# Kernel optimization log

Measured on AMD Instinct MI355X. Metric: run time of the kernel, lower is better.

The kernel has to match this reference:

```python
import jax, jax.numpy as jnp
import numpy as np

E = 8          # num experts
TOPK = 2
D = 1024       # emb_size (expert hidden == emb_size)


def setup_inputs() -> dict:
    key = jax.random.key(0)
    ks = jax.random.split(key, 8)
    s = 1.0 / np.sqrt(D)
    x = jax.random.normal(ks[0], (4, 1024, D), dtype=jnp.float32)
    gate_W = jax.random.uniform(ks[1], (E, D), jnp.float32, -s, s)   # torch Linear weight (out,in)
    gate_b = jax.random.uniform(ks[2], (E,), jnp.float32, -s, s)
    w1 = jax.random.uniform(ks[3], (E, D, D), jnp.float32, -s, s)    # per-expert first Linear (out,in)
    b1 = jax.random.uniform(ks[4], (E, D), jnp.float32, -s, s)
    w2 = jax.random.uniform(ks[5], (E, D, D), jnp.float32, -s, s)    # per-expert second Linear (out,in)
    b2 = jax.random.uniform(ks[6], (E, D), jnp.float32, -s, s)
    return {"x": x, "gate_W": gate_W, "gate_b": gate_b,
            "w1": w1, "b1": b1, "w2": w2, "b2": b2}


def reference(x, gate_W, gate_b, w1, b1, w2, b2):
    x_shape = x.shape
    xt = x.reshape(-1, x_shape[-1])                       # [N, D]

    # gating
    gate_logits = xt @ gate_W.T + gate_b                  # [N, E]
    gate_prob = jax.nn.softmax(gate_logits, axis=-1)      # [N, E]
    top_w, top_i = jax.lax.top_k(gate_prob, TOPK)         # [N, K]
    top_w = jax.nn.softmax(top_w, axis=-1)                # renormalize over top-k

    # dense per-expert MLP: h = relu(x @ W1^T + b1); o = h @ W2^T + b2
    h = jax.nn.relu(jnp.einsum('nd,ehd->neh', xt, w1) + b1[None])   # [N, E, D]
    o = jnp.einsum('neh,eoh->neo', h, w2) + b2[None]                # [N, E, D]

    # gather top-k expert outputs per token and combine with weights
    o_top = jnp.take_along_axis(o, top_i[:, :, None], axis=1)       # [N, K, D]
    y = jnp.sum(o_top * top_w[:, :, None], axis=1)                  # [N, D]

    return y.reshape(x_shape), gate_prob
```

## Files before the change

### kernel.cpp

```cpp
#include <hip/hip_runtime.h>

#define NTOK 4096
#define DIM 1024
#define NE 8
#define NPAIR (NTOK * 2)

typedef __bf16 bf16x8 __attribute__((ext_vector_type(8)));
typedef float floatx4 __attribute__((ext_vector_type(4)));

__device__ __forceinline__ unsigned short f2bf(float f) {
  unsigned u = __float_as_uint(f);
  u = u + 0x7fffu + ((u >> 16) & 1u);
  return (unsigned short)(u >> 16);
}
__device__ __forceinline__ float bf2f(unsigned short h) {
  return __uint_as_float(((unsigned)h) << 16);
}

__device__ __forceinline__ void gld_lds16(const unsigned short* g, unsigned short* l) {
  __builtin_amdgcn_global_load_lds(
      (const __attribute__((address_space(1))) void*)g,
      (__attribute__((address_space(3))) void*)l, 16, 0, 0);
}

__global__ __launch_bounds__(256) void gate_kernel(
    const float* __restrict__ x, const float* __restrict__ gW,
    const float* __restrict__ gb,
    float* __restrict__ gp_out, int2* __restrict__ tops,
    float* __restrict__ pairw, int* __restrict__ cnt, int* __restrict__ done,
    unsigned short* __restrict__ x_bf)
{
  const int tid = threadIdx.x;
  if (blockIdx.x == 0) {
    if (tid < NE) cnt[tid] = 0;
    if (tid == NE) *done = 0;
  }
  const int lane = tid & 63;
  const int wid = tid >> 6;
  const int t = blockIdx.x * 4 + wid;

  float4 xv[4];
#pragma unroll
  for (int j = 0; j < 4; j++)
    xv[j] = ((const float4*)(x + (size_t)t * DIM))[lane + 64 * j];

#pragma unroll
  for (int j = 0; j < 4; j++) {
    ushort4 o;
    o.x = f2bf(xv[j].x); o.y = f2bf(xv[j].y);
    o.z = f2bf(xv[j].z); o.w = f2bf(xv[j].w);
    ((ushort4*)(x_bf + (size_t)t * DIM))[lane + 64 * j] = o;
  }

  float p[NE];
#pragma unroll
  for (int e = 0; e < NE; e++) {
    const float4* gwe = (const float4*)(gW + e * DIM);
    float s = 0.f;
#pragma unroll
    for (int j = 0; j < 4; j++) {
      float4 g = gwe[lane + 64 * j];
      s += xv[j].x * g.x + xv[j].y * g.y + xv[j].z * g.z + xv[j].w * g.w;
    }
    p[e] = s;
  }
#pragma unroll
  for (int e = 0; e < NE; e++) {
#pragma unroll
    for (int off = 32; off >= 1; off >>= 1) p[e] += __shfl_xor(p[e], off);
  }

  float m = -1e30f;
#pragma unroll
  for (int e = 0; e < NE; e++) { p[e] += gb[e]; m = fmaxf(m, p[e]); }
  float s = 0.f;
  float pr[NE];
#pragma unroll
  for (int e = 0; e < NE; e++) { pr[e] = __expf(p[e] - m); s += pr[e]; }
  float inv = 1.f / s;
#pragma unroll
  for (int e = 0; e < NE; e++) pr[e] *= inv;

  if (lane < NE) gp_out[(size_t)t * NE + lane] = pr[lane];

  if (lane == 0) {
    int i0 = 0;
#pragma unroll
    for (int e = 1; e < NE; e++) if (pr[e] > pr[i0]) i0 = e;
    int i1 = (i0 == 0) ? 1 : 0;
#pragma unroll
    for (int e = 0; e < NE; e++) if (e != i0 && pr[e] > pr[i1]) i1 = e;
    float d = __expf(pr[i1] - pr[i0]);
    float w0 = 1.f / (1.f + d);
    tops[t] = make_int2(i0, i1);
    pairw[t * 2] = w0;
    pairw[t * 2 + 1] = 1.f - w0;
  }
}

__global__ __launch_bounds__(256) void bin_sched_kernel(
    const int2* __restrict__ tops, int* __restrict__ cnt,
    int* __restrict__ bucket,
    int* __restrict__ posmap,
    int* __restrict__ done, int* __restrict__ base,
    int* __restrict__ sched, int* __restrict__ sched_n)
{
  const int t = blockIdx.x * 256 + threadIdx.x;
  const int lane = threadIdx.x & 63;
  int2 ti = tops[t];
#pragma unroll
  for (int slot = 0; slot < 2; slot++) {
    int e = slot ? ti.y : ti.x;
#pragma unroll
    for (int ex = 0; ex < NE; ex++) {
      bool mine = (e == ex);
      unsigned long long mask = __ballot(mine);
      if (mask) {
        int leader = __ffsll((long long)mask) - 1;
        int total = __popcll(mask);
        int prefix = __popcll(mask & ((1ull << lane) - 1ull));
        int idx = 0;
        if (lane == leader) idx = atomicAdd(&cnt[ex], total);
        idx = __shfl(idx, leader) + prefix;
        if (mine) {
          bucket[ex * NTOK + idx] = t * 2 + slot;
          posmap[t * 2 + slot] = (ex << 16) | idx;
        }
      }
    }
  }
  __syncthreads();
  if (threadIdx.x == 0) {
    if (atomicAdd(done, 1) == gridDim.x - 1) {
      int b = 0, pos = 0;
      for (int e = 0; e < NE; e++) {
        int c = atomicAdd(&cnt[e], 0);
        base[e] = b;
        int tiles = (c + 127) >> 7;
        for (int i = 0; i < tiles; i++) {
          int valid = c - i * 128; if (valid > 128) valid = 128;
          sched[pos++] = (e << 20) | (i << 8) | valid;
        }
        b += c;
      }
      base[NE] = b;
      *sched_n = pos;
    }
  }
}

__global__ __launch_bounds__(256) void cvt2_kernel(
    const float4* __restrict__ src1, ushort4* __restrict__ dst1,
    const float4* __restrict__ src2, ushort4* __restrict__ dst2, int half_blocks)
{
  int b = blockIdx.x;
  const float4* src = src1;
  ushort4* dst = dst1;
  if (b >= half_blocks) { b -= half_blocks; src = src2; dst = dst2; }
  const int i = b * 256 + threadIdx.x;
  float4 v = src[i];
  ushort4 o;
  o.x = f2bf(v.x); o.y = f2bf(v.y); o.z = f2bf(v.z); o.w = f2bf(v.w);
  dst[i] = o;
}

template <int RELU, int GATHER>
__global__ __launch_bounds__(512) void ffn_gemm(
    const unsigned short* __restrict__ A,
    const unsigned short* __restrict__ B,
    const float* __restrict__ bias,
    const int* __restrict__ base,
    const int* __restrict__ bucket,
    const int* __restrict__ sched, const int* __restrict__ sched_n,
    unsigned short* __restrict__ Out)
{
  const int l = blockIdx.x;
  const int xcd = l & 7;
  const int w = l >> 3;
  const int nt = w & 7;
  const int slot = xcd * 9 + (w >> 3);
  if (slot >= *sched_n) return;
  const int se = sched[slot];
  const int e = se >> 20;
  const int mt = (se >> 8) & 0xfff;
  const int valid = se & 255;
  const int arow0 = base[e] + mt * 128;

  __shared__ unsigned short lda[128 * 64];
  __shared__ unsigned short ldb[128 * 64];

  const int tid = threadIdx.x;
  const int lane = tid & 63;
  const int wid = tid >> 6;

  const unsigned short* ap[2];
  const unsigned short* bp[2];
#pragma unroll
  for (int j = 0; j < 2; j++) {
    int g = wid * 2 + j;
    int row = g * 8 + (lane >> 3);
    int gran = (lane & 7) ^ (row & 7);
    if (GATHER) {
      int idx = mt * 128 + row;
      int ce = base[e + 1] - base[e];
      if (idx > ce - 1) idx = ce - 1;
      int tok = bucket[e * NTOK + idx] >> 1;
      ap[j] = A + (size_t)tok * DIM + (gran << 3);
    } else {
      int prow = arow0 + row;
      if (prow > NPAIR - 1) prow = NPAIR - 1;
      ap[j] = A + (size_t)prow * DIM + (gran << 3);
    }
    bp[j] = B + ((size_t)e * DIM + nt * 128 + row) * DIM + (gran << 3);
  }

  floatx4 acc[4][2] = {};
  const int wm = (wid & 1) * 64;
  const int wn = (wid >> 1) * 32;
  const int quad = lane >> 4;
  const int cl = lane & 15;
  const int sw = cl & 7;

  for (int k0 = 0; k0 < 16; k0++) {
#pragma unroll
    for (int j = 0; j < 2; j++) {
      gld_lds16(ap[j], &lda[(wid * 2 + j) * 512]);
      gld_lds16(bp[j], &ldb[(wid * 2 + j) * 512]);
      ap[j] += 64;
      bp[j] += 64;
    }
    __syncthreads();
#pragma unroll
    for (int kk = 0; kk < 64; kk += 32) {
      const int gb = (kk >> 3) + quad;
      const int goff = ((gb ^ sw) << 3);
      bf16x8 af[4], bfr[2];
#pragma unroll
      for (int mi = 0; mi < 4; mi++)
        af[mi] = *(const bf16x8*)&lda[(wm + mi * 16 + cl) * 64 + goff];
#pragma unroll
      for (int ni = 0; ni < 2; ni++)
        bfr[ni] = *(const bf16x8*)&ldb[(wn + ni * 16 + cl) * 64 + goff];
#pragma unroll
      for (int mi = 0; mi < 4; mi++)
#pragma unroll
        for (int ni = 0; ni < 2; ni++)
          acc[mi][ni] = __builtin_amdgcn_mfma_f32_16x16x32_bf16(af[mi], bfr[ni], acc[mi][ni], 0, 0, 0);
    }
    if (k0 < 15) __syncthreads();
  }

#pragma unroll
  for (int ni = 0; ni < 2; ni++) {
    int col = nt * 128 + wn + ni * 16 + cl;
    float bval = bias[e * DIM + col];
#pragma unroll
    for (int mi = 0; mi < 4; mi++) {
#pragma unroll
      for (int reg = 0; reg < 4; reg++) {
        int rl = wm + mi * 16 + quad * 4 + reg;
        if (rl < valid) {
          float v = acc[mi][ni][reg] + bval;
          if (RELU) v = fmaxf(v, 0.f);
          Out[(size_t)(arow0 + rl) * DIM + col] = f2bf(v);
        }
      }
    }
  }
}

__global__ __launch_bounds__(256) void combine_kernel(
    const unsigned short* __restrict__ o, const int* __restrict__ posmap,
    const int* __restrict__ base, const float* __restrict__ pairw,
    float* __restrict__ y)
{
  const int t = blockIdx.x;
  const int tid = threadIdx.x;
  const int pm0 = posmap[t * 2], pm1 = posmap[t * 2 + 1];
  const int p0 = base[pm0 >> 16] + (pm0 & 0xffff);
  const int p1 = base[pm1 >> 16] + (pm1 & 0xffff);
  const float w0 = pairw[t * 2], w1 = pairw[t * 2 + 1];
  ushort4 a = ((const ushort4*)(o + (size_t)p0 * DIM))[tid];
  ushort4 b = ((const ushort4*)(o + (size_t)p1 * DIM))[tid];
  float4 r;
  r.x = w0 * bf2f(a.x) + w1 * bf2f(b.x);
  r.y = w0 * bf2f(a.y) + w1 * bf2f(b.y);
  r.z = w0 * bf2f(a.z) + w1 * bf2f(b.z);
  r.w = w0 * bf2f(a.w) + w1 * bf2f(b.w);
  ((float4*)(y + (size_t)t * DIM))[tid] = r;
}

extern "C" void kernel_launch(void* const* d_in, const int* in_sizes, int n_in,
                              void* d_out, int out_size, void* d_ws, size_t ws_size,
                              hipStream_t stream) {
  const float* x  = (const float*)d_in[0];
  const float* gW = (const float*)d_in[1];
  const float* gb = (const float*)d_in[2];
  const float* w1 = (const float*)d_in[3];
  const float* b1 = (const float*)d_in[4];
  const float* w2 = (const float*)d_in[5];
  const float* b2 = (const float*)d_in[6];
  float* y  = (float*)d_out;
  float* gp = (float*)d_out + (size_t)NTOK * DIM;

  char* ws = (char*)d_ws;
  unsigned short* x_bf   = (unsigned short*)(ws);
  unsigned short* w2_bf  = (unsigned short*)(ws + (size_t)(8u << 20));
  unsigned short* h_pack = (unsigned short*)(ws + (size_t)(24u << 20));
  unsigned short* w1_bf  = (unsigned short*)(ws + (size_t)(40u << 20));
  unsigned short* o_pack = (unsigned short*)(ws + (size_t)(40u << 20));
  char* tail = ws + (size_t)(56u << 20);
  int*   cnt     = (int*)(tail);
  int*   done    = cnt + NE;
  int*   base    = done + 1;
  int*   sched   = base + NE + 1;
  int*   sched_n = sched + 256;
  int*   bucket  = sched_n + 1;
  float* pairw   = (float*)(bucket + NE * NTOK);
  int2*  tops    = (int2*)(pairw + NPAIR);
  int*   posmap  = (int*)(tops + NTOK);

  const int cvt_half = (NE * DIM * DIM / 4) / 256;
  const int gemm_grid = 576;
  cvt2_kernel<<<cvt_half * 2, 256, 0, stream>>>((const float4*)w1, (ushort4*)w1_bf,
                                                (const float4*)w2, (ushort4*)w2_bf, cvt_half);
  gate_kernel<<<NTOK / 4, 256, 0, stream>>>(x, gW, gb, gp, tops, pairw, cnt, done, x_bf);
  bin_sched_kernel<<<NTOK / 256, 256, 0, stream>>>(tops, cnt, bucket, posmap, done,
                                                   base, sched, sched_n);
  ffn_gemm<1, 1><<<gemm_grid, 512, 0, stream>>>(x_bf, w1_bf, b1, base, bucket, sched, sched_n, h_pack);
  ffn_gemm<0, 0><<<gemm_grid, 512, 0, stream>>>(h_pack, w2_bf, b2, base, bucket, sched, sched_n, o_pack);
  combine_kernel<<<NTOK, 256, 0, stream>>>(o_pack, posmap, base, pairw, y);
}
```

Before: 222.0 us.

## Fuse weight conversion with gating and use 4-wave GEMM blocks with 64x64 warp tiles

Merges the fp32-to-bf16 weight conversion kernel into the gating kernel as one launch, with block ranges dispatching to either role. The expert GEMMs now use 256-thread blocks where each wave computes a 64x64 subtile with 16 accumulators and issues 4 load groups per K step. This improves register-level reuse of LDS fragments and removes a launch, at the cost of more registers per wave and fewer waves to hide load latency.

```diff
diff --git a/kernel.cpp b/kernel.cpp
--- a/kernel.cpp
+++ b/kernel.cpp
@@ -4,6 +4,8 @@
 #define DIM 1024
 #define NE 8
 #define NPAIR (NTOK * 2)
+#define CVT_BLOCKS 16384
+#define GATE_BLOCKS (NTOK / 4)
 
 typedef __bf16 bf16x8 __attribute__((ext_vector_type(8)));
 typedef float floatx4 __attribute__((ext_vector_type(4)));
@@ -23,7 +25,9 @@
       (__attribute__((address_space(3))) void*)l, 16, 0, 0);
 }
 
-__global__ __launch_bounds__(256) void gate_kernel(
+__global__ __launch_bounds__(256) void prep_kernel(
+    const float4* __restrict__ w1, ushort4* __restrict__ w1_bf,
+    const float4* __restrict__ w2, ushort4* __restrict__ w2_bf,
     const float* __restrict__ x, const float* __restrict__ gW,
     const float* __restrict__ gb,
     float* __restrict__ gp_out, int2* __restrict__ tops,
@@ -31,13 +35,26 @@
     unsigned short* __restrict__ x_bf)
 {
   const int tid = threadIdx.x;
-  if (blockIdx.x == 0) {
+  int b = blockIdx.x;
+  if (b < CVT_BLOCKS) {
+    const float4* src = w1;
+    ushort4* dst = w1_bf;
+    if (b >= CVT_BLOCKS / 2) { b -= CVT_BLOCKS / 2; src = w2; dst = w2_bf; }
+    const int i = b * 256 + tid;
+    float4 v = src[i];
+    ushort4 o;
+    o.x = f2bf(v.x); o.y = f2bf(v.y); o.z = f2bf(v.z); o.w = f2bf(v.w);
+    dst[i] = o;
+    return;
+  }
+  b -= CVT_BLOCKS;
+  if (b == 0) {
     if (tid < NE) cnt[tid] = 0;
     if (tid == NE) *done = 0;
   }
   const int lane = tid & 63;
   const int wid = tid >> 6;
-  const int t = blockIdx.x * 4 + wid;
+  const int t = b * 4 + wid;
 
   float4 xv[4];
 #pragma unroll
@@ -149,23 +166,8 @@
   }
 }
 
-__global__ __launch_bounds__(256) void cvt2_kernel(
-    const float4* __restrict__ src1, ushort4* __restrict__ dst1,
-    const float4* __restrict__ src2, ushort4* __restrict__ dst2, int half_blocks)
-{
-  int b = blockIdx.x;
-  const float4* src = src1;
-  ushort4* dst = dst1;
-  if (b >= half_blocks) { b -= half_blocks; src = src2; dst = dst2; }
-  const int i = b * 256 + threadIdx.x;
-  float4 v = src[i];
-  ushort4 o;
-  o.x = f2bf(v.x); o.y = f2bf(v.y); o.z = f2bf(v.z); o.w = f2bf(v.w);
-  dst[i] = o;
-}
-
 template <int RELU, int GATHER>
-__global__ __launch_bounds__(512) void ffn_gemm(
+__global__ __launch_bounds__(256) void ffn_gemm(
     const unsigned short* __restrict__ A,
     const unsigned short* __restrict__ B,
     const float* __restrict__ bias,
@@ -193,11 +195,11 @@
   const int lane = tid & 63;
   const int wid = tid >> 6;
 
-  const unsigned short* ap[2];
-  const unsigned short* bp[2];
-#pragma unroll
-  for (int j = 0; j < 2; j++) {
-    int g = wid * 2 + j;
+  const unsigned short* ap[4];
+  const unsigned short* bp[4];
+#pragma unroll
+  for (int j = 0; j < 4; j++) {
+    int g = wid * 4 + j;
     int row = g * 8 + (lane >> 3);
     int gran = (lane & 7) ^ (row & 7);
     if (GATHER) {
@@ -214,18 +216,19 @@
     bp[j] = B + ((size_t)e * DIM + nt * 128 + row) * DIM + (gran << 3);
   }
 
-  floatx4 acc[4][2] = {};
+  floatx4 acc[4][4] = {};
   const int wm = (wid & 1) * 64;
-  const int wn = (wid >> 1) * 32;
+  const int wn = (wid >> 1) * 64;
   const int quad = lane >> 4;
   const int cl = lane & 15;
   const int sw = cl & 7;
 
   for (int k0 = 0; k0 < 16; k0++) {
 #pragma unroll
-    for (int j = 0; j < 2; j++) {
-      gld_lds16(ap[j], &lda[(wid * 2 + j) * 512]);
-      gld_lds16(bp[j], &ldb[(wid * 2 + j) * 512]);
+    for (int j = 0; j < 4; j++) {
+      int g = wid * 4 + j;
+      gld_lds16(ap[j], &lda[g * 512]);
+      gld_lds16(bp[j], &ldb[g * 512]);
       ap[j] += 64;
       bp[j] += 64;
     }
@@ -234,24 +237,24 @@
     for (int kk = 0; kk < 64; kk += 32) {
       const int gb = (kk >> 3) + quad;
       const int goff = ((gb ^ sw) << 3);
-      bf16x8 af[4], bfr[2];
+      bf16x8 af[4], bfr[4];
 #pragma unroll
       for (int mi = 0; mi < 4; mi++)
         af[mi] = *(const bf16x8*)&lda[(wm + mi * 16 + cl) * 64 + goff];
 #pragma unroll
-      for (int ni = 0; ni < 2; ni++)
+      for (int ni = 0; ni < 4; ni++)
         bfr[ni] = *(const bf16x8*)&ldb[(wn + ni * 16 + cl) * 64 + goff];
 #pragma unroll
       for (int mi = 0; mi < 4; mi++)
 #pragma unroll
-        for (int ni = 0; ni < 2; ni++)
+        for (int ni = 0; ni < 4; ni++)
           acc[mi][ni] = __builtin_amdgcn_mfma_f32_16x16x32_bf16(af[mi], bfr[ni], acc[mi][ni], 0, 0, 0);
     }
     if (k0 < 15) __syncthreads();
   }
 
 #pragma unroll
-  for (int ni = 0; ni < 2; ni++) {
+  for (int ni = 0; ni < 4; ni++) {
     int col = nt * 128 + wn + ni * 16 + cl;
     float bval = bias[e * DIM + col];
 #pragma unroll
@@ -320,14 +323,13 @@
   int2*  tops    = (int2*)(pairw + NPAIR);
   int*   posmap  = (int*)(tops + NTOK);
 
-  const int cvt_half = (NE * DIM * DIM / 4) / 256;
   const int gemm_grid = 576;
-  cvt2_kernel<<<cvt_half * 2, 256, 0, stream>>>((const float4*)w1, (ushort4*)w1_bf,
-                                                (const float4*)w2, (ushort4*)w2_bf, cvt_half);
-  gate_kernel<<<NTOK / 4, 256, 0, stream>>>(x, gW, gb, gp, tops, pairw, cnt, done, x_bf);
+  prep_kernel<<<CVT_BLOCKS + GATE_BLOCKS, 256, 0, stream>>>(
+      (const float4*)w1, (ushort4*)w1_bf, (const float4*)w2, (ushort4*)w2_bf,
+      x, gW, gb, gp, tops, pairw, cnt, done, x_bf);
   bin_sched_kernel<<<NTOK / 256, 256, 0, stream>>>(tops, cnt, bucket, posmap, done,
                                                    base, sched, sched_n);
-  ffn_gemm<1, 1><<<gemm_grid, 512, 0, stream>>>(x_bf, w1_bf, b1, base, bucket, sched, sched_n, h_pack);
-  ffn_gemm<0, 0><<<gemm_grid, 512, 0, stream>>>(h_pack, w2_bf, b2, base, bucket, sched, sched_n, o_pack);
+  ffn_gemm<1, 1><<<gemm_grid, 256, 0, stream>>>(x_bf, w1_bf, b1, base, bucket, sched, sched_n, h_pack);
+  ffn_gemm<0, 0><<<gemm_grid, 256, 0, stream>>>(h_pack, w2_bf, b2, base, bucket, sched, sched_n, o_pack);
   combine_kernel<<<NTOK, 256, 0, stream>>>(o_pack, posmap, base, pairw, y);
 }
```

Result: slower. 228.9 us (+3.1%).
